# Kernel tuning notes

Hardware: AMD Instinct MI355X
Metric: run time of the kernel (lower is better)

## Reference

```python
import jax, jax.numpy as jnp
import numpy as np

N = 4096
IN_C = 256
F = 256          # num_filter
C = 40           # label_dim
KP1 = 3          # K+1 Chebyshev orders (K=2 hardcoded in forward)
E = 131072
TWO_PI = 2.0 * np.pi


def build_Lc(edges, q, edge_weight, n):
    """Conjugate of the normalized magnetic Laplacian (max_eigen=2 => L = -A_n * exp(i*Theta)).
    We return conj(L) because the original code swaps L.real/L.imag when feeding `process`,
    which is algebraically O_i = i * conj(T_i(L))."""
    row, col = edges[0], edges[1]
    A = jnp.zeros((n, n), jnp.float32).at[row, col].add(edge_weight)  # duplicates sum, as in coo_matrix
    A_sym = 0.5 * (A + A.T)
    d = A_sym.sum(axis=0)
    d = jnp.where(d == 0, 1.0, d)
    dinv = d ** -0.5
    A_n = dinv[:, None] * A_sym * dinv[None, :]
    Theta = TWO_PI * q * (A - A.T)
    # conj(L) = -A_n * exp(-i*Theta)
    return (-A_n).astype(jnp.complex64) * jnp.exp(-1j * Theta.astype(jnp.complex64))


def cheb_layer(Lc, Xr, Xi, W, b):
    """One ChebConv_Qin_Direct layer. Output = sum_i (i * T_i(conj(L)) @ Xc) @ W_i + bias,
    which reproduces the real/imag-swapped `process` of the original module."""
    Xc = (Xr + 1j * Xi).astype(jnp.complex64)      # [N, d]
    Z0 = Xc
    Z1 = Lc @ Xc                                   # sparse-equivalent spmm, dense here
    Z2 = 2.0 * (Lc @ Z1) - Z0                      # Chebyshev recursion T2 = 2 L T1 - T0
    Yc = 1j * (Z0 @ W[0].astype(jnp.complex64)
               + Z1 @ W[1].astype(jnp.complex64)
               + Z2 @ W[2].astype(jnp.complex64))  # [N, out]
    return Yc.real + b, Yc.imag + b


def setup_inputs() -> dict:
    key = jax.random.key(0)
    k = jax.random.split(key, 8)
    stdv1 = 1.0 / np.sqrt(F)
    return {
        "real": jax.random.normal(k[0], (N, IN_C), jnp.float32),
        "imag": jax.random.normal(k[1], (N, IN_C), jnp.float32),
        "edges": jax.random.randint(k[2], (2, E), 0, N),
        "q": jnp.float32(0.25),
        "edge_weight": jax.random.uniform(k[3], (E,), jnp.float32),
        "W1": jax.random.uniform(k[4], (KP1, IN_C, F), jnp.float32, -stdv1, stdv1),
        "b1": jnp.zeros((1, F), jnp.float32),
        "W2": jax.random.uniform(k[5], (KP1, F, F), jnp.float32, -stdv1, stdv1),
        "b2": jnp.zeros((1, F), jnp.float32),
        "Wc": jax.random.normal(k[6], (C, 2 * F), jnp.float32) * (1.0 / np.sqrt(2 * F)),
        "bc": jnp.zeros((C,), jnp.float32),
    }


def reference(real, imag, edges, q, edge_weight, W1, b1, W2, b2, Wc, bc):
    n = real.shape[0]
    Lc = build_Lc(edges, q, edge_weight, n)        # same L is rebuilt each layer in the original
    r, i = cheb_layer(Lc, real, imag, W1, b1)
    r, i = cheb_layer(Lc, r, i, W2, b2)            # activation=False, dropout=False
    x = jnp.concatenate([r, i], axis=-1)           # [N, 2F]
    logits = x @ Wc.T + bc                         # Conv1d(kernel_size=1) == linear
    return jax.nn.log_softmax(logits, axis=-1)     # [N, C]
```

## Files before the change

kernel.cpp:

```cpp
#include <hip/hip_runtime.h>
#include <cmath>

#define N_NODES 4096
#define FDIM    256
#define CDIM    40
#define NEDGE   131072
#define CAP     256
#define HBITS   20
#define HSIZE   (1 << HBITS)
#define TWO_PI_F 6.28318530717958647692f
#define NWT     (256 * 768)

typedef __bf16 bf16;
typedef __bf16 bf16x2 __attribute__((ext_vector_type(2)));
typedef __bf16 bf16x4 __attribute__((ext_vector_type(4)));
typedef __bf16 bf16x8 __attribute__((ext_vector_type(8)));
typedef float  f32x4  __attribute__((ext_vector_type(4)));

static constexpr size_t NF = (size_t)N_NODES * FDIM;
static constexpr int ZWORDS = 2 * HSIZE + 3 * N_NODES;

struct __align__(16) Entry { float lr, li; int col, pad; };

struct Params {
    const int* edges; const float* ew; const float* q;
    const float* real; const float* imag;
    const float* W1; const float* b1; const float* W2; const float* b2;
    const float* Wc; const float* bc;
    int* hkey; float* hval; int* cnt; float* rowsum; float* colsum;
    Entry* ent;
    bf16 *Xr16, *Xi16, *XC;
    bf16 *Z1r, *Z1i, *Z1C, *Z2r, *Z2i;
    bf16 *Y1rb, *Y1ib, *Y1C, *Y2rb, *Y2ib;
    bf16 *W1t, *W2t, *Wcb;
    float* out;
};

__device__ __forceinline__ void gld_lds16(const bf16* g, bf16* s) {
    __builtin_amdgcn_global_load_lds(
        (const __attribute__((address_space(1))) void*)g,
        (__attribute__((address_space(3))) void*)s,
        16, 0, 0);
}

__device__ __forceinline__ unsigned cell_hash(unsigned cell) {
    return (cell * 2654435761u) >> (32 - HBITS);
}

__device__ void init_stage(const Params& p, int gtid, int stride) {
    int* zw = (int*)p.hkey;
    for (int w0 = gtid; w0 < ZWORDS; w0 += stride) zw[w0] = 0;

    for (int idx = gtid; idx < (int)NF; idx += stride) {
        float vr = p.real[idx], vi = p.imag[idx];
        p.Xr16[idx] = (bf16)vr; p.Xi16[idx] = (bf16)vi;
        bf16x2 pp; pp[0] = (bf16)vr; pp[1] = (bf16)vi;
        ((bf16x2*)p.XC)[idx] = pp;
    }
    for (int idx = gtid; idx < 2 * NWT + 48 * 512; idx += stride) {
        if (idx < 2 * NWT) {
            const float* W = (idx < NWT) ? p.W1 : p.W2;
            bf16* Wt = (idx < NWT) ? p.W1t : p.W2t;
            int id = (idx < NWT) ? idx : idx - NWT;
            int nout = id / 768, kk = id - nout * 768;
            int o = kk >> 8, k = kk & 255;
            Wt[id] = (bf16)W[((size_t)o * 256 + k) * 256 + nout];
        } else {
            int id = idx - 2 * NWT;
            int row = id >> 9, k = id & 511;
            p.Wcb[id] = (row < CDIM) ? (bf16)p.Wc[row * 512 + k] : (bf16)0.f;
        }
    }
}

__device__ void hash_stage(const Params& p, int gtid, int stride) {
    for (int e = gtid; e < NEDGE; e += stride) {
        int r = p.edges[e], c = p.edges[NEDGE + e];
        float wv = p.ew[e];
        atomicAdd(p.rowsum + r, wv);
        atomicAdd(p.colsum + c, wv);
        unsigned cell = (unsigned)r * N_NODES + c;
        unsigned h = cell_hash(cell);
        for (;;) {
            int old = atomicCAS(p.hkey + h, 0, (int)(cell + 1));
            if (old == 0 || old == (int)(cell + 1)) { atomicAdd(p.hval + h, wv); break; }
            h = (h + 1) & (HSIZE - 1);
        }
    }
}

__device__ void ell_stage(const Params& p, int gtid, int stride) {
    for (int h = gtid; h < HSIZE; h += stride) {
        int k = p.hkey[h];
        if (k == 0) continue;
        unsigned cell = (unsigned)(k - 1);
        int i = cell >> 12, j = cell & 4095;
        float a = p.hval[h];
        float b = 0.f;
        bool mirror = false;
        if (i == j) { b = a; mirror = true; }
        else {
            unsigned mcell = (unsigned)j * N_NODES + i;
            unsigned hh = cell_hash(mcell);
            for (;;) {
                int kk = p.hkey[hh];
                if (kk == (int)(mcell + 1)) { b = p.hval[hh]; mirror = true; break; }
                if (kk == 0) break;
                hh = (hh + 1) & (HSIZE - 1);
            }
        }
        float di = 0.5f * (p.rowsum[i] + p.colsum[i]); if (di == 0.f) di = 1.f;
        float dj = 0.5f * (p.rowsum[j] + p.colsum[j]); if (dj == 0.f) dj = 1.f;
        float an = 0.5f * (a + b) / sqrtf(di * dj);
        float s, c;
        sincosf(TWO_PI_F * p.q[0] * (a - b), &s, &c);
        int pos = atomicAdd(p.cnt + i, 1);
        if (pos < CAP) {
            Entry en; en.lr = -an * c; en.li = an * s; en.col = j; en.pad = 0;
            p.ent[(size_t)i * CAP + pos] = en;
        }
        if (!mirror) {
            int pos2 = atomicAdd(p.cnt + j, 1);
            if (pos2 < CAP) {
                Entry en; en.lr = -an * c; en.li = -an * s; en.col = i; en.pad = 0;
                p.ent[(size_t)j * CAP + pos2] = en;
            }
        }
    }
}

__device__ void spmm_stage(const int* __restrict__ cnt, const Entry* __restrict__ ent,
                           const bf16* __restrict__ XC, const bf16* __restrict__ C0C,
                           float alpha, float beta,
                           bf16* __restrict__ Zr, bf16* __restrict__ Zi,
                           bf16* __restrict__ ZC, char* smem, int bid, int nblocks)
{
    f32x4* redR = (f32x4*)smem;
    f32x4* redI = redR + 192;
    const int wave = threadIdx.x >> 6, lane = threadIdx.x & 63;

    for (int row = bid; row < N_NODES; row += nblocks) {
        int n1 = cnt[row]; if (n1 > CAP) n1 = CAP;
        const Entry* erow = ent + (size_t)row * CAP;

        float ar[4] = {}, ai[4] = {};
        int e = wave;
        for (; e + 12 < n1; e += 16) {
            Entry e0 = erow[e];
            Entry e1 = erow[e + 4];
            Entry e2 = erow[e + 8];
            Entry e3 = erow[e + 12];
            bf16x8 x0 = *(const bf16x8*)&XC[(size_t)(e0.col & 4095) * 512 + lane * 8];
            bf16x8 x1 = *(const bf16x8*)&XC[(size_t)(e1.col & 4095) * 512 + lane * 8];
            bf16x8 x2 = *(const bf16x8*)&XC[(size_t)(e2.col & 4095) * 512 + lane * 8];
            bf16x8 x3 = *(const bf16x8*)&XC[(size_t)(e3.col & 4095) * 512 + lane * 8];
            #pragma unroll
            for (int c = 0; c < 4; ++c) {
                float xr, xi;
                xr = (float)x0[2 * c]; xi = (float)x0[2 * c + 1];
                ar[c] += e0.lr * xr - e0.li * xi;  ai[c] += e0.lr * xi + e0.li * xr;
                xr = (float)x1[2 * c]; xi = (float)x1[2 * c + 1];
                ar[c] += e1.lr * xr - e1.li * xi;  ai[c] += e1.lr * xi + e1.li * xr;
                xr = (float)x2[2 * c]; xi = (float)x2[2 * c + 1];
                ar[c] += e2.lr * xr - e2.li * xi;  ai[c] += e2.lr * xi + e2.li * xr;
                xr = (float)x3[2 * c]; xi = (float)x3[2 * c + 1];
                ar[c] += e3.lr * xr - e3.li * xi;  ai[c] += e3.lr * xi + e3.li * xr;
            }
        }
        for (; e < n1; e += 4) {
            Entry e0 = erow[e];
            bf16x8 x0 = *(const bf16x8*)&XC[(size_t)(e0.col & 4095) * 512 + lane * 8];
            #pragma unroll
            for (int c = 0; c < 4; ++c) {
                float xr0 = (float)x0[2 * c], xi0 = (float)x0[2 * c + 1];
                ar[c] += e0.lr * xr0 - e0.li * xi0;
                ai[c] += e0.lr * xi0 + e0.li * xr0;
            }
        }

        if (wave != 0) {
            f32x4 r, i;
            #pragma unroll
            for (int c = 0; c < 4; ++c) { r[c] = ar[c]; i[c] = ai[c]; }
            redR[(wave - 1) * 64 + lane] = r;
            redI[(wave - 1) * 64 + lane] = i;
        }
        __syncthreads();
        if (wave == 0) {
            #pragma unroll
            for (int w = 0; w < 3; ++w) {
                f32x4 r = redR[w * 64 + lane], i = redI[w * 64 + lane];
                #pragma unroll
                for (int c = 0; c < 4; ++c) { ar[c] += r[c]; ai[c] += i[c]; }
            }
            float vr[4], vi[4];
            if (beta != 0.f) {
                bf16x8 c0 = *(const bf16x8*)&C0C[(size_t)row * 512 + lane * 8];
                #pragma unroll
                for (int c = 0; c < 4; ++c) {
                    vr[c] = alpha * ar[c] + beta * (float)c0[2 * c];
                    vi[c] = alpha * ai[c] + beta * (float)c0[2 * c + 1];
                }
            } else {
                #pragma unroll
                for (int c = 0; c < 4; ++c) { vr[c] = alpha * ar[c]; vi[c] = alpha * ai[c]; }
            }
            size_t base = (size_t)row * FDIM + lane * 4;
            bf16x4 pr, pi;
            #pragma unroll
            for (int c = 0; c < 4; ++c) { pr[c] = (bf16)vr[c]; pi[c] = (bf16)vi[c]; }
            *(bf16x4*)&Zr[base] = pr;
            *(bf16x4*)&Zi[base] = pi;
            if (ZC) {
                bf16x8 o;
                #pragma unroll
                for (int c = 0; c < 4; ++c) { o[2 * c] = pr[c]; o[2 * c + 1] = pi[c]; }
                *(bf16x8*)&ZC[(size_t)row * 512 + lane * 8] = o;
            }
        }
        __syncthreads();
    }
}

__device__ void wapply_stage(const bf16* __restrict__ Z0r, const bf16* __restrict__ Z0i,
                             const bf16* __restrict__ Z1r, const bf16* __restrict__ Z1i,
                             const bf16* __restrict__ Z2r, const bf16* __restrict__ Z2i,
                             const bf16* __restrict__ Wt, const float* __restrict__ bias,
                             bf16* __restrict__ Or, bf16* __restrict__ Oi,
                             bf16* __restrict__ OC, char* smem, int bid, int nblocks)
{
    bf16* sZr = (bf16*)smem;
    bf16* sZi = (bf16*)(smem + 4096);
    bf16* sW  = (bf16*)(smem + 8192);

    const int tid  = threadIdx.x;
    const int wave = tid >> 6;
    const int lane = tid & 63;
    const int wm = wave & 1, wn = wave >> 1;
    const int fr = lane & 15;
    const int fk = (lane >> 4) * 8;
    const int srow = lane >> 2;
    const int skc  = (lane & 3) * 8;

    for (int tile = bid; tile < 256; tile += nblocks) {
        const int rowBase = (tile >> 2) * 64;
        const int colBase = (tile & 3) * 64;

        f32x4 accSr[2][2] = {}, accSi[2][2] = {};

        for (int kb = 0; kb < 3 * FDIM; kb += 32) {
            int order = kb >> 8;
            int kloc  = kb & 255;
            if (wave == 0 || wave == 1) {
                const bf16* z;
                if (wave == 0) z = (order == 0) ? Z0r : (order == 1) ? Z1r : Z2r;
                else           z = (order == 0) ? Z0i : (order == 1) ? Z1i : Z2i;
                bf16* s = (wave == 0) ? sZr : sZi;
                const bf16* g = z + (size_t)(rowBase + srow) * FDIM + kloc + skc;
                #pragma unroll
                for (int t = 0; t < 4; ++t)
                    gld_lds16(g + (size_t)t * 16 * FDIM, s + t * 512);
            } else if (wave == 2) {
                const bf16* g = Wt + (size_t)(colBase + srow) * 768 + kb + skc;
                #pragma unroll
                for (int t = 0; t < 4; ++t)
                    gld_lds16(g + (size_t)t * 16 * 768, sW + t * 512);
            }
            __syncthreads();

            bf16x8 zr[2], zi[2], wv[2];
            #pragma unroll
            for (int m = 0; m < 2; ++m) {
                int r = wm * 32 + m * 16 + fr;
                zr[m] = *(const bf16x8*)&sZr[r * 32 + fk];
                zi[m] = *(const bf16x8*)&sZi[r * 32 + fk];
            }
            #pragma unroll
            for (int n = 0; n < 2; ++n) {
                int c = wn * 32 + n * 16 + fr;
                wv[n] = *(const bf16x8*)&sW[c * 32 + fk];
            }
            #pragma unroll
            for (int m = 0; m < 2; ++m)
                #pragma unroll
                for (int n = 0; n < 2; ++n) {
                    accSr[m][n] = __builtin_amdgcn_mfma_f32_16x16x32_bf16(zr[m], wv[n], accSr[m][n], 0, 0, 0);
                    accSi[m][n] = __builtin_amdgcn_mfma_f32_16x16x32_bf16(zi[m], wv[n], accSi[m][n], 0, 0, 0);
                }
            __syncthreads();
        }

        #pragma unroll
        for (int m = 0; m < 2; ++m)
            #pragma unroll
            for (int n = 0; n < 2; ++n) {
                int row0 = rowBase + wm * 32 + m * 16 + (lane >> 4) * 4;
                int col  = colBase + wn * 32 + n * 16 + (lane & 15);
                float bv = bias[col];
                #pragma unroll
                for (int r = 0; r < 4; ++r) {
                    float vr = bv - accSi[m][n][r];
                    float vi = bv + accSr[m][n][r];
                    size_t idx = (size_t)(row0 + r) * FDIM + col;
                    Or[idx] = (bf16)vr; Oi[idx] = (bf16)vi;
                    if (OC) {
                        bf16x2 pp; pp[0] = (bf16)vr; pp[1] = (bf16)vi;
                        ((bf16x2*)OC)[idx] = pp;
                    }
                }
            }
    }
}

__device__ void head_stage(const bf16* __restrict__ Yrb, const bf16* __restrict__ Yib,
                           const bf16* __restrict__ Wcb, const float* __restrict__ bc,
                           float* __restrict__ out, char* smem, int bid, int nblocks)
{
    bf16*  sY = (bf16*)smem;
    bf16*  sW = (bf16*)(smem + 9216);
    float* sS = (float*)smem;

    const int tid  = threadIdx.x;
    const int wave = tid >> 6;
    const int lane = tid & 63;

    for (int t0 = bid; t0 < 64; t0 += nblocks) {
        const int r0 = t0 * 64;
        f32x4 acc[3] = {};

        for (int kb = 0; kb < 512; kb += 64) {
            const bf16* src = (kb < 256) ? Yrb : Yib;
            const int koff = kb & 255;
            #pragma unroll
            for (int e = 0; e < 2; ++e) {
                int idx = tid + e * 256;
                int rr = idx >> 3, kk = (idx & 7) * 8;
                *(bf16x8*)&sY[rr * 72 + kk] =
                    *(const bf16x8*)&src[(size_t)(r0 + rr) * FDIM + koff + kk];
            }
            #pragma unroll
            for (int e = 0; e < 2; ++e) {
                int idx = tid + e * 256;
                if (idx < 384) {
                    int rr = idx >> 3, kk = (idx & 7) * 8;
                    *(bf16x8*)&sW[rr * 72 + kk] =
                        *(const bf16x8*)&Wcb[(size_t)rr * 512 + kb + kk];
                }
            }
            __syncthreads();
            #pragma unroll
            for (int ks = 0; ks < 2; ++ks) {
                bf16x8 a = *(const bf16x8*)&sY[(wave * 16 + (lane & 15)) * 72 + ks * 32 + (lane >> 4) * 8];
                #pragma unroll
                for (int n = 0; n < 3; ++n) {
                    bf16x8 b = *(const bf16x8*)&sW[(n * 16 + (lane & 15)) * 72 + ks * 32 + (lane >> 4) * 8];
                    acc[n] = __builtin_amdgcn_mfma_f32_16x16x32_bf16(a, b, acc[n], 0, 0, 0);
                }
            }
            __syncthreads();
        }

        #pragma unroll
        for (int n = 0; n < 3; ++n) {
            int col = n * 16 + (lane & 15);
            int rloc = wave * 16 + (lane >> 4) * 4;
            #pragma unroll
            for (int r = 0; r < 4; ++r)
                sS[(rloc + r) * 52 + col] = acc[n][r];
        }
        __syncthreads();

        if (tid < 64) {
            float mx = -INFINITY;
            #pragma unroll 8
            for (int c = 0; c < CDIM; ++c) {
                float lv = sS[tid * 52 + c] + bc[c];
                sS[tid * 52 + c] = lv;
                mx = fmaxf(mx, lv);
            }
            float se = 0.f;
            #pragma unroll 8
            for (int c = 0; c < CDIM; ++c) se += expf(sS[tid * 52 + c] - mx);
            float lse = mx + logf(se);
            #pragma unroll 8
            for (int c = 0; c < CDIM; ++c)
                out[(size_t)(r0 + tid) * CDIM + c] = sS[tid * 52 + c] - lse;
        }
        __syncthreads();
    }
}

__global__ __launch_bounds__(256) void k_init(Params p) {
    init_stage(p, blockIdx.x * 256 + threadIdx.x, gridDim.x * 256);
}
__global__ __launch_bounds__(256) void k_hash(Params p) {
    hash_stage(p, blockIdx.x * 256 + threadIdx.x, gridDim.x * 256);
}
__global__ __launch_bounds__(256) void k_ell(Params p) {
    ell_stage(p, blockIdx.x * 256 + threadIdx.x, gridDim.x * 256);
}
__global__ __launch_bounds__(256) void k_spmm(const int* cnt, const Entry* ent,
                                              const bf16* XC, const bf16* C0C,
                                              float alpha, float beta,
                                              bf16* Zr, bf16* Zi, bf16* ZC) {
    __shared__ __align__(16) char smem[6144];
    spmm_stage(cnt, ent, XC, C0C, alpha, beta, Zr, Zi, ZC, smem, blockIdx.x, gridDim.x);
}
__global__ __launch_bounds__(256) void k_wapply(const bf16* Z0r, const bf16* Z0i,
                                                const bf16* Z1r, const bf16* Z1i,
                                                const bf16* Z2r, const bf16* Z2i,
                                                const bf16* Wt, const float* bias,
                                                bf16* Or, bf16* Oi, bf16* OC) {
    __shared__ __align__(16) char smem[12288];
    wapply_stage(Z0r, Z0i, Z1r, Z1i, Z2r, Z2i, Wt, bias, Or, Oi, OC, smem,
                 blockIdx.x, gridDim.x);
}
__global__ __launch_bounds__(256) void k_head(const bf16* Yrb, const bf16* Yib,
                                              const bf16* Wcb, const float* bc,
                                              float* out) {
    __shared__ __align__(16) char smem[16384];
    head_stage(Yrb, Yib, Wcb, bc, out, smem, blockIdx.x, gridDim.x);
}

extern "C" void kernel_launch(void* const* d_in, const int* in_sizes, int n_in,
                              void* d_out, int out_size, void* d_ws, size_t ws_size,
                              hipStream_t stream) {
    Params p;
    p.real = (const float*)d_in[0];
    p.imag = (const float*)d_in[1];
    p.edges = (const int*)d_in[2];
    p.q    = (const float*)d_in[3];
    p.ew   = (const float*)d_in[4];
    p.W1   = (const float*)d_in[5];
    p.b1   = (const float*)d_in[6];
    p.W2   = (const float*)d_in[7];
    p.b2   = (const float*)d_in[8];
    p.Wc   = (const float*)d_in[9];
    p.bc   = (const float*)d_in[10];
    p.out  = (float*)d_out;

    char* w = (char*)d_ws;
    p.hkey   = (int*)w;   w += (size_t)HSIZE * 4;
    p.hval   = (float*)w; w += (size_t)HSIZE * 4;
    p.cnt    = (int*)w;   w += N_NODES * 4;
    p.rowsum = (float*)w; w += N_NODES * 4;
    p.colsum = (float*)w; w += N_NODES * 4;
    p.ent    = (Entry*)w; w += (size_t)N_NODES * CAP * 16;
    p.Xr16 = (bf16*)w; w += NF * 2;
    p.Xi16 = (bf16*)w; w += NF * 2;
    p.XC   = (bf16*)w; w += NF * 4;
    p.Z1r  = (bf16*)w; w += NF * 2;
    p.Z1i  = (bf16*)w; w += NF * 2;
    p.Z1C  = (bf16*)w; w += NF * 4;
    p.Z2r  = (bf16*)w; w += NF * 2;
    p.Z2i  = (bf16*)w; w += NF * 2;
    p.Y1rb = (bf16*)w; w += NF * 2;
    p.Y1ib = (bf16*)w; w += NF * 2;
    p.Y1C  = (bf16*)w; w += NF * 4;
    p.Y2rb = (bf16*)w; w += NF * 2;
    p.Y2ib = (bf16*)w; w += NF * 2;
    p.W1t  = (bf16*)w; w += 256 * 768 * 2;
    p.W2t  = (bf16*)w; w += 256 * 768 * 2;
    p.Wcb  = (bf16*)w; w += 48 * 512 * 2;

    dim3 b(256);
    k_init<<<512, b, 0, stream>>>(p);
    k_hash<<<512, b, 0, stream>>>(p);
    k_ell<<<512, b, 0, stream>>>(p);
    k_spmm<<<4096, b, 0, stream>>>(p.cnt, p.ent, p.XC, nullptr,
                                   1.f, 0.f, p.Z1r, p.Z1i, p.Z1C);
    k_spmm<<<4096, b, 0, stream>>>(p.cnt, p.ent, p.Z1C, p.XC,
                                   2.f, -1.f, p.Z2r, p.Z2i, nullptr);
    k_wapply<<<256, b, 0, stream>>>(p.Xr16, p.Xi16, p.Z1r, p.Z1i, p.Z2r, p.Z2i,
                                    p.W1t, p.b1, p.Y1rb, p.Y1ib, p.Y1C);
    k_spmm<<<4096, b, 0, stream>>>(p.cnt, p.ent, p.Y1C, nullptr,
                                   1.f, 0.f, p.Z1r, p.Z1i, p.Z1C);
    k_spmm<<<4096, b, 0, stream>>>(p.cnt, p.ent, p.Z1C, p.Y1C,
                                   2.f, -1.f, p.Z2r, p.Z2i, nullptr);
    k_wapply<<<256, b, 0, stream>>>(p.Y1rb, p.Y1ib, p.Z1r, p.Z1i, p.Z2r, p.Z2i,
                                    p.W2t, p.b2, p.Y2rb, p.Y2ib, nullptr);
    k_head<<<64, b, 0, stream>>>(p.Y2rb, p.Y2ib, p.Wcb, p.bc, p.out);
}
```

Before: 282.0 us.

## Split interleaved complex feature buffers into two half-feature planes for SpMM

Stores the interleaved complex bf16 features as two planes of 128 features each, so each SpMM block handles one (row, half) pair and the grid doubles to 8192 blocks. Each gathered neighbour row is now a contiguous 512-byte slice within a smaller plane, which should improve cache locality of the random gathers and give more parallelism. The cost is that every block re-reads the ELL entry list for its row, per-lane loads shrink to 8 bytes, and the reduction and sync overhead per output doubles.

```diff
diff --git a/kernel.cpp b/kernel.cpp
--- a/kernel.cpp
+++ b/kernel.cpp
@@ -10,6 +10,7 @@
 #define HSIZE   (1 << HBITS)
 #define TWO_PI_F 6.28318530717958647692f
 #define NWT     (256 * 768)
+#define HPLANE  ((size_t)N_NODES * 256)
 
 typedef __bf16 bf16;
 typedef __bf16 bf16x2 __attribute__((ext_vector_type(2)));
@@ -55,7 +56,9 @@
         float vr = p.real[idx], vi = p.imag[idx];
         p.Xr16[idx] = (bf16)vr; p.Xi16[idx] = (bf16)vi;
         bf16x2 pp; pp[0] = (bf16)vr; pp[1] = (bf16)vi;
-        ((bf16x2*)p.XC)[idx] = pp;
+        int n = idx >> 8, f = idx & 255;
+        int h = f >> 7, fl = f & 127;
+        *(bf16x2*)&p.XC[(size_t)h * HPLANE + (size_t)n * 256 + fl * 2] = pp;
     }
     for (int idx = gtid; idx < 2 * NWT + 48 * 512; idx += stride) {
         if (idx < 2 * NWT) {
@@ -130,32 +133,35 @@
 }
 
 __device__ void spmm_stage(const int* __restrict__ cnt, const Entry* __restrict__ ent,
-                           const bf16* __restrict__ XC, const bf16* __restrict__ C0C,
+                           const bf16* __restrict__ XCh, const bf16* __restrict__ C0h,
                            float alpha, float beta,
                            bf16* __restrict__ Zr, bf16* __restrict__ Zi,
-                           bf16* __restrict__ ZC, char* smem, int bid, int nblocks)
+                           bf16* __restrict__ ZCh, char* smem, int bid, int nblocks)
 {
-    f32x4* redR = (f32x4*)smem;
-    f32x4* redI = redR + 192;
+    float2* redR = (float2*)smem;
+    float2* redI = redR + 192;
     const int wave = threadIdx.x >> 6, lane = threadIdx.x & 63;
 
-    for (int row = bid; row < N_NODES; row += nblocks) {
+    for (int t = bid; t < 2 * N_NODES; t += nblocks) {
+        const int h   = t & 1;
+        const int row = t >> 1;
+        const bf16* Xp = XCh + (size_t)h * HPLANE;
         int n1 = cnt[row]; if (n1 > CAP) n1 = CAP;
         const Entry* erow = ent + (size_t)row * CAP;
 
-        float ar[4] = {}, ai[4] = {};
+        float ar[2] = {}, ai[2] = {};
         int e = wave;
         for (; e + 12 < n1; e += 16) {
             Entry e0 = erow[e];
             Entry e1 = erow[e + 4];
             Entry e2 = erow[e + 8];
             Entry e3 = erow[e + 12];
-            bf16x8 x0 = *(const bf16x8*)&XC[(size_t)(e0.col & 4095) * 512 + lane * 8];
-            bf16x8 x1 = *(const bf16x8*)&XC[(size_t)(e1.col & 4095) * 512 + lane * 8];
-            bf16x8 x2 = *(const bf16x8*)&XC[(size_t)(e2.col & 4095) * 512 + lane * 8];
-            bf16x8 x3 = *(const bf16x8*)&XC[(size_t)(e3.col & 4095) * 512 + lane * 8];
-            #pragma unroll
-            for (int c = 0; c < 4; ++c) {
+            bf16x4 x0 = *(const bf16x4*)&Xp[(size_t)(e0.col & 4095) * 256 + lane * 4];
+            bf16x4 x1 = *(const bf16x4*)&Xp[(size_t)(e1.col & 4095) * 256 + lane * 4];
+            bf16x4 x2 = *(const bf16x4*)&Xp[(size_t)(e2.col & 4095) * 256 + lane * 4];
+            bf16x4 x3 = *(const bf16x4*)&Xp[(size_t)(e3.col & 4095) * 256 + lane * 4];
+            #pragma unroll
+            for (int c = 0; c < 2; ++c) {
                 float xr, xi;
                 xr = (float)x0[2 * c]; xi = (float)x0[2 * c + 1];
                 ar[c] += e0.lr * xr - e0.li * xi;  ai[c] += e0.lr * xi + e0.li * xr;
@@ -169,9 +175,9 @@
         }
         for (; e < n1; e += 4) {
             Entry e0 = erow[e];
-            bf16x8 x0 = *(const bf16x8*)&XC[(size_t)(e0.col & 4095) * 512 + lane * 8];
-            #pragma unroll
-            for (int c = 0; c < 4; ++c) {
+            bf16x4 x0 = *(const bf16x4*)&Xp[(size_t)(e0.col & 4095) * 256 + lane * 4];
+            #pragma unroll
+            for (int c = 0; c < 2; ++c) {
                 float xr0 = (float)x0[2 * c], xi0 = (float)x0[2 * c + 1];
                 ar[c] += e0.lr * xr0 - e0.li * xi0;
                 ai[c] += e0.lr * xi0 + e0.li * xr0;
@@ -179,43 +185,39 @@
         }
 
         if (wave != 0) {
-            f32x4 r, i;
-            #pragma unroll
-            for (int c = 0; c < 4; ++c) { r[c] = ar[c]; i[c] = ai[c]; }
-            redR[(wave - 1) * 64 + lane] = r;
-            redI[(wave - 1) * 64 + lane] = i;
+            redR[(wave - 1) * 64 + lane] = make_float2(ar[0], ar[1]);
+            redI[(wave - 1) * 64 + lane] = make_float2(ai[0], ai[1]);
         }
         __syncthreads();
         if (wave == 0) {
             #pragma unroll
             for (int w = 0; w < 3; ++w) {
-                f32x4 r = redR[w * 64 + lane], i = redI[w * 64 + lane];
-                #pragma unroll
-                for (int c = 0; c < 4; ++c) { ar[c] += r[c]; ai[c] += i[c]; }
-            }
-            float vr[4], vi[4];
+                float2 r = redR[w * 64 + lane], i = redI[w * 64 + lane];
+                ar[0] += r.x; ar[1] += r.y;
+                ai[0] += i.x; ai[1] += i.y;
+            }
+            float vr[2], vi[2];
             if (beta != 0.f) {
-                bf16x8 c0 = *(const bf16x8*)&C0C[(size_t)row * 512 + lane * 8];
-                #pragma unroll
-                for (int c = 0; c < 4; ++c) {
+                bf16x4 c0 = *(const bf16x4*)&C0h[(size_t)h * HPLANE + (size_t)row * 256 + lane * 4];
+                #pragma unroll
+                for (int c = 0; c < 2; ++c) {
                     vr[c] = alpha * ar[c] + beta * (float)c0[2 * c];
                     vi[c] = alpha * ai[c] + beta * (float)c0[2 * c + 1];
                 }
             } else {
                 #pragma unroll
-                for (int c = 0; c < 4; ++c) { vr[c] = alpha * ar[c]; vi[c] = alpha * ai[c]; }
-            }
-            size_t base = (size_t)row * FDIM + lane * 4;
-            bf16x4 pr, pi;
-            #pragma unroll
-            for (int c = 0; c < 4; ++c) { pr[c] = (bf16)vr[c]; pi[c] = (bf16)vi[c]; }
-            *(bf16x4*)&Zr[base] = pr;
-            *(bf16x4*)&Zi[base] = pi;
-            if (ZC) {
-                bf16x8 o;
-                #pragma unroll
-                for (int c = 0; c < 4; ++c) { o[2 * c] = pr[c]; o[2 * c + 1] = pi[c]; }
-                *(bf16x8*)&ZC[(size_t)row * 512 + lane * 8] = o;
+                for (int c = 0; c < 2; ++c) { vr[c] = alpha * ar[c]; vi[c] = alpha * ai[c]; }
+            }
+            size_t pbase = (size_t)row * FDIM + h * 128 + lane * 2;
+            bf16x2 pr, pi;
+            pr[0] = (bf16)vr[0]; pr[1] = (bf16)vr[1];
+            pi[0] = (bf16)vi[0]; pi[1] = (bf16)vi[1];
+            *(bf16x2*)&Zr[pbase] = pr;
+            *(bf16x2*)&Zi[pbase] = pi;
+            if (ZCh) {
+                bf16x4 o;
+                o[0] = pr[0]; o[1] = pi[0]; o[2] = pr[1]; o[3] = pi[1];
+                *(bf16x4*)&ZCh[(size_t)h * HPLANE + (size_t)row * 256 + lane * 4] = o;
             }
         }
         __syncthreads();
@@ -304,8 +306,9 @@
                     size_t idx = (size_t)(row0 + r) * FDIM + col;
                     Or[idx] = (bf16)vr; Oi[idx] = (bf16)vi;
                     if (OC) {
+                        int hh = col >> 7, fl = col & 127;
                         bf16x2 pp; pp[0] = (bf16)vr; pp[1] = (bf16)vi;
-                        ((bf16x2*)OC)[idx] = pp;
+                        *(bf16x2*)&OC[(size_t)hh * HPLANE + (size_t)(row0 + r) * 256 + fl * 2] = pp;
                     }
                 }
             }
@@ -400,11 +403,11 @@
     ell_stage(p, blockIdx.x * 256 + threadIdx.x, gridDim.x * 256);
 }
 __global__ __launch_bounds__(256) void k_spmm(const int* cnt, const Entry* ent,
-                                              const bf16* XC, const bf16* C0C,
+                                              const bf16* XCh, const bf16* C0h,
                                               float alpha, float beta,
-                                              bf16* Zr, bf16* Zi, bf16* ZC) {
-    __shared__ __align__(16) char smem[6144];
-    spmm_stage(cnt, ent, XC, C0C, alpha, beta, Zr, Zi, ZC, smem, blockIdx.x, gridDim.x);
+                                              bf16* Zr, bf16* Zi, bf16* ZCh) {
+    __shared__ __align__(16) char smem[3072];
+    spmm_stage(cnt, ent, XCh, C0h, alpha, beta, Zr, Zi, ZCh, smem, blockIdx.x, gridDim.x);
 }
 __global__ __launch_bounds__(256) void k_wapply(const bf16* Z0r, const bf16* Z0i,
                                                 const bf16* Z1r, const bf16* Z1i,
@@ -467,15 +470,15 @@
     k_init<<<512, b, 0, stream>>>(p);
     k_hash<<<512, b, 0, stream>>>(p);
     k_ell<<<512, b, 0, stream>>>(p);
-    k_spmm<<<4096, b, 0, stream>>>(p.cnt, p.ent, p.XC, nullptr,
+    k_spmm<<<8192, b, 0, stream>>>(p.cnt, p.ent, p.XC, nullptr,
                                    1.f, 0.f, p.Z1r, p.Z1i, p.Z1C);
-    k_spmm<<<4096, b, 0, stream>>>(p.cnt, p.ent, p.Z1C, p.XC,
+    k_spmm<<<8192, b, 0, stream>>>(p.cnt, p.ent, p.Z1C, p.XC,
                                    2.f, -1.f, p.Z2r, p.Z2i, nullptr);
     k_wapply<<<256, b, 0, stream>>>(p.Xr16, p.Xi16, p.Z1r, p.Z1i, p.Z2r, p.Z2i,
                                     p.W1t, p.b1, p.Y1rb, p.Y1ib, p.Y1C);
-    k_spmm<<<4096, b, 0, stream>>>(p.cnt, p.ent, p.Y1C, nullptr,
+    k_spmm<<<8192, b, 0, stream>>>(p.cnt, p.ent, p.Y1C, nullptr,
                                    1.f, 0.f, p.Z1r, p.Z1i, p.Z1C);
-    k_spmm<<<4096, b, 0, stream>>>(p.cnt, p.ent, p.Z1C, p.Y1C,
+    k_spmm<<<8192, b, 0, stream>>>(p.cnt, p.ent, p.Z1C, p.Y1C,
                                    2.f, -1.f, p.Z2r, p.Z2i, nullptr);
     k_wapply<<<256, b, 0, stream>>>(p.Y1rb, p.Y1ib, p.Z1r, p.Z1i, p.Z2r, p.Z2i,
                                     p.W2t, p.b2, p.Y2rb, p.Y2ib, nullptr);
```

New measurement: 318.8 us. 13.1% more time.
